# Optimization experiments

Hardware: AMD Instinct MI355X
Metric: run time of the kernel (lower is better)

The kernel has to match this reference:

```python
import jax, jax.numpy as jnp
import numpy as np

NUM_BREAKPOINTS = 100  # module default
IMG_SHAPE = (1, 1, 4096, 8192)  # B must be 1: PWL(num_channels=1) sees (C*H*W, B)


def setup_inputs() -> dict:
    key = jax.random.key(0)
    k1, k2, k3, k4 = jax.random.split(key, 4)
    x = jax.random.uniform(k1, IMG_SHAPE, dtype=jnp.float32)
    # torchpwl.PWL parameters (num_channels=1): breakpoint x-positions, per-segment
    # slopes, and bias (function value at the leftmost breakpoint).
    x_positions = jax.random.uniform(k2, (1, NUM_BREAKPOINTS), dtype=jnp.float32)
    slopes = 1.0 + 0.1 * jax.random.normal(k3, (1, NUM_BREAKPOINTS), dtype=jnp.float32)
    biases = 0.05 * jax.random.normal(k4, (1,), dtype=jnp.float32)
    return {"x": x, "x_positions": x_positions, "slopes": slopes, "biases": biases}


def _pwl(x_flat, x_positions, slopes, biases):
    # Sloped piecewise-linear function (torchpwl.BaseSlopedPWL math), 1 channel.
    # x_flat: (N,), x_positions/slopes: (1, K), biases: (1,)
    K = x_positions.shape[1]
    sorted_x = jnp.sort(x_positions, axis=1)                     # (1, K)
    skips = jnp.roll(sorted_x, -1, axis=1) - sorted_x            # last entry never used
    cumsums = jnp.cumsum(skips * slopes, axis=1)[:, :-1]         # (1, K-1)
    betas = jnp.concatenate([biases[:, None], biases[:, None] + cumsums], axis=1)  # (1, K)
    # segment index: (# breakpoints <= x) clamped to [1, K], minus 1
    idx = jnp.clip(jnp.searchsorted(sorted_x[0], x_flat, side="right"), 1, K) - 1
    return betas[0, idx] + (x_flat - sorted_x[0, idx]) * slopes[0, idx]


def reference(x, x_positions, slopes, biases):
    # forward: flatten -> PWL -> clip(0,1) -> reshape (original returns [out])
    y = _pwl(x.reshape(-1), x_positions, slopes, biases)
    return jnp.clip(y, 0.0, 1.0).reshape(x.shape)
```

## Files before the change

### kernel.cpp

```cpp
#include <hip/hip_runtime.h>

#define K  100
#define NB 1024

typedef float fvec4 __attribute__((ext_vector_type(4)));

__global__ __launch_bounds__(1024) void pwl_setup_kernel(
    const float* __restrict__ xp, const float* __restrict__ sl,
    const float* __restrict__ bias, float* __restrict__ a_g,
    float* __restrict__ b_g, float* __restrict__ sx_g,
    float2* __restrict__ ab_g) {
  __shared__ float s_pos[K];
  __shared__ float s_slope[K];
  __shared__ float s_x[K];
  __shared__ float s_c[K];
  __shared__ float s_sa[K];
  __shared__ float s_sb[K];
  __shared__ unsigned short s_cnt[NB + 1];
  const int t = threadIdx.x;

  if (t < K) { s_pos[t] = xp[t]; s_slope[t] = sl[t]; }
  __syncthreads();

  if (t < K) {
    float v = s_pos[t];
    int r = 0;
    for (int j = 0; j < K; ++j) {
      float u = s_pos[j];
      r += ((u < v) || (u == v && j < t)) ? 1 : 0;
    }
    s_x[r] = v;
  }
  __syncthreads();

  if (t < K - 1) s_c[t] = (s_x[t + 1] - s_x[t]) * s_slope[t];
  __syncthreads();
  for (int off = 1; off < K - 1; off <<= 1) {
    float v = 0.0f;
    if (t >= off && t < K - 1) v = s_c[t - off];
    __syncthreads();
    if (t < K - 1) s_c[t] += v;
    __syncthreads();
  }
  if (t < K) {
    float beta = bias[0] + (t ? s_c[t - 1] : 0.0f);
    float a = s_slope[t];
    s_sa[t] = a;
    s_sb[t] = beta - s_x[t] * a;
  }
  __syncthreads();

  if (t < K) {
    sx_g[t] = s_x[t];
    ab_g[t] = make_float2(s_sa[t], s_sb[t]);
  }

  for (int e = t; e <= NB; e += blockDim.x) {
    float ev = (float)e * (1.0f / (float)NB);
    int lo = 0, hi = K;
    while (lo < hi) {
      int mid = (lo + hi) >> 1;
      if (s_x[mid] <= ev) lo = mid + 1; else hi = mid;
    }
    s_cnt[e] = (unsigned short)lo;
  }
  __syncthreads();

  for (int b = t; b < NB; b += blockDim.x) {
    int lo = s_cnt[b], hi = s_cnt[b + 1];
    float av, bv;
    if (lo == hi) {
      int idx = min(max(lo, 1), K) - 1;
      av = s_sa[idx];
      bv = s_sb[idx];
    } else {
      av = __builtin_huge_valf();
      bv = __uint_as_float((unsigned)lo | ((unsigned)hi << 16));
    }
    a_g[b] = av;
    b_g[b] = bv;
  }
}

__device__ __forceinline__ float pwl_eval(float xv,
                                          const float* __restrict__ s_a,
                                          const float* __restrict__ s_b,
                                          const float* __restrict__ s_x,
                                          const float2* __restrict__ s_ab) {
  int bkt = (int)(xv * (float)NB);
  bkt = min(max(bkt, 0), NB - 1);
  float a = s_a[bkt];
  float b = s_b[bkt];
  if (__float_as_uint(a) == 0x7f800000u) {
    unsigned p = __float_as_uint(b);
    int lo = (int)(p & 0xffffu);
    int hi = (int)(p >> 16);
    while (lo < hi) {
      int mid = (lo + hi) >> 1;
      if (s_x[mid] <= xv) lo = mid + 1; else hi = mid;
    }
    int idx = min(max(lo, 1), K) - 1;
    float2 ab = s_ab[idx];
    a = ab.x;
    b = ab.y;
  }
  float y = fmaf(xv, a, b);
  return fminf(fmaxf(y, 0.0f), 1.0f);
}

__global__ __launch_bounds__(256) void pwl_main_kernel(
    const fvec4* __restrict__ x, const float* __restrict__ a_g,
    const float* __restrict__ b_g, const float* __restrict__ sx_g,
    const float2* __restrict__ ab_g, fvec4* __restrict__ out, int n4, int n) {
  __shared__ float s_a[NB];
  __shared__ float s_b[NB];
  __shared__ float s_x[K];
  __shared__ float2 s_ab[K];
  for (int i = threadIdx.x; i < NB; i += blockDim.x) {
    s_a[i] = a_g[i];
    s_b[i] = b_g[i];
  }
  if (threadIdx.x < K) {
    s_x[threadIdx.x] = sx_g[threadIdx.x];
    s_ab[threadIdx.x] = ab_g[threadIdx.x];
  }
  __syncthreads();

  const int stride = gridDim.x * blockDim.x;
  int i = blockIdx.x * blockDim.x + threadIdx.x;
  if (i < n4) {
    fvec4 v = x[i];
    while (true) {
      int inext = i + stride;
      bool more = inext < n4;
      fvec4 vn = {};
      if (more) vn = x[inext];
      fvec4 r;
      r.x = pwl_eval(v.x, s_a, s_b, s_x, s_ab);
      r.y = pwl_eval(v.y, s_a, s_b, s_x, s_ab);
      r.z = pwl_eval(v.z, s_a, s_b, s_x, s_ab);
      r.w = pwl_eval(v.w, s_a, s_b, s_x, s_ab);
      __builtin_nontemporal_store(r, &out[i]);
      if (!more) break;
      v = vn;
      i = inext;
    }
  }

  if (blockIdx.x == 0) {
    const float* xs = (const float*)x;
    float* os = (float*)out;
    for (int j = (n4 << 2) + threadIdx.x; j < n; j += blockDim.x) {
      os[j] = pwl_eval(xs[j], s_a, s_b, s_x, s_ab);
    }
  }
}

extern "C" void kernel_launch(void* const* d_in, const int* in_sizes, int n_in,
                              void* d_out, int out_size, void* d_ws, size_t ws_size,
                              hipStream_t stream) {
  const float* x    = (const float*)d_in[0];
  const float* xp   = (const float*)d_in[1];
  const float* sl   = (const float*)d_in[2];
  const float* bias = (const float*)d_in[3];
  float* out = (float*)d_out;

  float* a_tab = (float*)d_ws;
  float* b_tab = (float*)((char*)d_ws + NB * 4);
  float* sx    = (float*)((char*)d_ws + NB * 8);
  float2* ab   = (float2*)((char*)d_ws + NB * 8 + 512);

  const int n  = in_sizes[0];
  const int n4 = n >> 2;

  pwl_setup_kernel<<<1, 1024, 0, stream>>>(xp, sl, bias, a_tab, b_tab, sx, ab);

  const int threads = 256;
  const int blocks  = 2048;
  pwl_main_kernel<<<blocks, threads, 0, stream>>>(
      (const fvec4*)x, a_tab, b_tab, sx, ab, (fvec4*)out, n4, n);
}
```

Measured before the change: 243.0 us.

## Replace bucket table with branch-free two-breakpoint lookup and double-buffer loads

Each bucket now stores up to two breakpoint positions plus a base index packed into the low mantissa bits, so most lookups resolve with two comparisons. A global binary search is the fallback only for buckets holding more than two breakpoints. The old version did a shared-memory binary search whenever a bucket held any breakpoint. The main loop also keeps two vec4 loads in flight per iteration to deepen memory-level parallelism. The price is a slight truncation of breakpoint precision in the low mantissa bits and extra register pressure.

```diff
diff --git a/kernel.cpp b/kernel.cpp
--- a/kernel.cpp
+++ b/kernel.cpp
@@ -7,9 +7,9 @@
 
 __global__ __launch_bounds__(1024) void pwl_setup_kernel(
     const float* __restrict__ xp, const float* __restrict__ sl,
-    const float* __restrict__ bias, float* __restrict__ a_g,
-    float* __restrict__ b_g, float* __restrict__ sx_g,
-    float2* __restrict__ ab_g) {
+    const float* __restrict__ bias, float* __restrict__ s0_g,
+    float* __restrict__ s1_g, float* __restrict__ sa_g,
+    float* __restrict__ sb_g, float* __restrict__ sx_g) {
   __shared__ float s_pos[K];
   __shared__ float s_slope[K];
   __shared__ float s_x[K];
@@ -51,8 +51,9 @@
   __syncthreads();
 
   if (t < K) {
+    sa_g[t] = s_sa[t];
+    sb_g[t] = s_sb[t];
     sx_g[t] = s_x[t];
-    ab_g[t] = make_float2(s_sa[t], s_sb[t]);
   }
 
   for (int e = t; e <= NB; e += blockDim.x) {
@@ -68,82 +69,118 @@
 
   for (int b = t; b < NB; b += blockDim.x) {
     int lo = s_cnt[b], hi = s_cnt[b + 1];
-    float av, bv;
-    if (lo == hi) {
-      int idx = min(max(lo, 1), K) - 1;
-      av = s_sa[idx];
-      bv = s_sb[idx];
-    } else {
-      av = __builtin_huge_valf();
-      bv = __uint_as_float((unsigned)lo | ((unsigned)hi << 16));
-    }
-    a_g[b] = av;
-    b_g[b] = bv;
-  }
-}
-
-__device__ __forceinline__ float pwl_eval(float xv,
-                                          const float* __restrict__ s_a,
-                                          const float* __restrict__ s_b,
-                                          const float* __restrict__ s_x,
-                                          const float2* __restrict__ s_ab) {
-  int bkt = (int)(xv * (float)NB);
-  bkt = min(max(bkt, 0), NB - 1);
-  float a = s_a[bkt];
-  float b = s_b[bkt];
-  if (__float_as_uint(a) == 0x7f800000u) {
-    unsigned p = __float_as_uint(b);
-    int lo = (int)(p & 0xffffu);
-    int hi = (int)(p >> 16);
-    while (lo < hi) {
-      int mid = (lo + hi) >> 1;
-      if (s_x[mid] <= xv) lo = mid + 1; else hi = mid;
-    }
-    int idx = min(max(lo, 1), K) - 1;
-    float2 ab = s_ab[idx];
-    a = ab.x;
-    b = ab.y;
-  }
-  float y = fmaf(xv, a, b);
-  return fminf(fmaxf(y, 0.0f), 1.0f);
+    int m = hi - lo;
+    float s0 = (m >= 1) ? s_x[lo] : __builtin_huge_valf();
+    float s1 = (m >= 2) ? s_x[lo + 1] : __builtin_huge_valf();
+    unsigned enc = (unsigned)lo | ((m > 2) ? 0x80u : 0u);
+    unsigned u = (__float_as_uint(s0) & 0xFFFFFF00u) | enc;
+    s0_g[b] = __uint_as_float(u);
+    s1_g[b] = s1;
+  }
+}
+
+__device__ __forceinline__ int pwl_gsearch(const float* __restrict__ sx,
+                                           float xv) {
+  int lo = 0, hi = K;
+  while (lo < hi) {
+    int mid = (lo + hi) >> 1;
+    if (sx[mid] <= xv) lo = mid + 1; else hi = mid;
+  }
+  return max(lo - 1, 0);
+}
+
+__device__ __forceinline__ fvec4 pwl_eval4(fvec4 v,
+    const float* __restrict__ s_s0, const float* __restrict__ s_s1,
+    const float* __restrict__ s_sa, const float* __restrict__ s_sb,
+    const float* __restrict__ sx_g) {
+  int b0 = min(max((int)(v.x * (float)NB), 0), NB - 1);
+  int b1 = min(max((int)(v.y * (float)NB), 0), NB - 1);
+  int b2 = min(max((int)(v.z * (float)NB), 0), NB - 1);
+  int b3 = min(max((int)(v.w * (float)NB), 0), NB - 1);
+  unsigned u0 = __float_as_uint(s_s0[b0]);
+  unsigned u1 = __float_as_uint(s_s0[b1]);
+  unsigned u2 = __float_as_uint(s_s0[b2]);
+  unsigned u3 = __float_as_uint(s_s0[b3]);
+  float t0 = s_s1[b0], t1 = s_s1[b1], t2 = s_s1[b2], t3 = s_s1[b3];
+  int i0 = max((int)(u0 & 0x7fu) + (int)(v.x >= __uint_as_float(u0)) + (int)(v.x >= t0) - 1, 0);
+  int i1 = max((int)(u1 & 0x7fu) + (int)(v.y >= __uint_as_float(u1)) + (int)(v.y >= t1) - 1, 0);
+  int i2 = max((int)(u2 & 0x7fu) + (int)(v.z >= __uint_as_float(u2)) + (int)(v.z >= t2) - 1, 0);
+  int i3 = max((int)(u3 & 0x7fu) + (int)(v.w >= __uint_as_float(u3)) + (int)(v.w >= t3) - 1, 0);
+  if (__builtin_expect(((u0 | u1 | u2 | u3) & 0x80u) != 0, 0)) {
+    if (u0 & 0x80u) i0 = pwl_gsearch(sx_g, v.x);
+    if (u1 & 0x80u) i1 = pwl_gsearch(sx_g, v.y);
+    if (u2 & 0x80u) i2 = pwl_gsearch(sx_g, v.z);
+    if (u3 & 0x80u) i3 = pwl_gsearch(sx_g, v.w);
+  }
+  float a0 = s_sa[i0], a1 = s_sa[i1], a2 = s_sa[i2], a3 = s_sa[i3];
+  float c0 = s_sb[i0], c1 = s_sb[i1], c2 = s_sb[i2], c3 = s_sb[i3];
+  fvec4 r;
+  r.x = fminf(fmaxf(fmaf(v.x, a0, c0), 0.0f), 1.0f);
+  r.y = fminf(fmaxf(fmaf(v.y, a1, c1), 0.0f), 1.0f);
+  r.z = fminf(fmaxf(fmaf(v.z, a2, c2), 0.0f), 1.0f);
+  r.w = fminf(fmaxf(fmaf(v.w, a3, c3), 0.0f), 1.0f);
+  return r;
+}
+
+__device__ __forceinline__ float pwl_eval1(float xv,
+    const float* __restrict__ s_s0, const float* __restrict__ s_s1,
+    const float* __restrict__ s_sa, const float* __restrict__ s_sb,
+    const float* __restrict__ sx_g) {
+  int b = min(max((int)(xv * (float)NB), 0), NB - 1);
+  unsigned u = __float_as_uint(s_s0[b]);
+  float t = s_s1[b];
+  int idx = max((int)(u & 0x7fu) + (int)(xv >= __uint_as_float(u)) + (int)(xv >= t) - 1, 0);
+  if (__builtin_expect((u & 0x80u) != 0, 0)) idx = pwl_gsearch(sx_g, xv);
+  return fminf(fmaxf(fmaf(xv, s_sa[idx], s_sb[idx]), 0.0f), 1.0f);
 }
 
 __global__ __launch_bounds__(256) void pwl_main_kernel(
-    const fvec4* __restrict__ x, const float* __restrict__ a_g,
-    const float* __restrict__ b_g, const float* __restrict__ sx_g,
-    const float2* __restrict__ ab_g, fvec4* __restrict__ out, int n4, int n) {
-  __shared__ float s_a[NB];
-  __shared__ float s_b[NB];
-  __shared__ float s_x[K];
-  __shared__ float2 s_ab[K];
+    const fvec4* __restrict__ x, const float* __restrict__ s0_g,
+    const float* __restrict__ s1_g, const float* __restrict__ sa_g,
+    const float* __restrict__ sb_g, const float* __restrict__ sx_g,
+    fvec4* __restrict__ out, int n4, int n) {
+  __shared__ float s_s0[NB];
+  __shared__ float s_s1[NB];
+  __shared__ float s_sa[K];
+  __shared__ float s_sb[K];
   for (int i = threadIdx.x; i < NB; i += blockDim.x) {
-    s_a[i] = a_g[i];
-    s_b[i] = b_g[i];
+    s_s0[i] = s0_g[i];
+    s_s1[i] = s1_g[i];
   }
   if (threadIdx.x < K) {
-    s_x[threadIdx.x] = sx_g[threadIdx.x];
-    s_ab[threadIdx.x] = ab_g[threadIdx.x];
+    s_sa[threadIdx.x] = sa_g[threadIdx.x];
+    s_sb[threadIdx.x] = sb_g[threadIdx.x];
   }
   __syncthreads();
 
   const int stride = gridDim.x * blockDim.x;
   int i = blockIdx.x * blockDim.x + threadIdx.x;
   if (i < n4) {
-    fvec4 v = x[i];
+    fvec4 v0 = x[i];
+    int i1 = i + stride;
+    bool h1 = i1 < n4;
+    fvec4 v1 = {};
+    if (h1) v1 = x[i1];
     while (true) {
-      int inext = i + stride;
-      bool more = inext < n4;
-      fvec4 vn = {};
-      if (more) vn = x[inext];
-      fvec4 r;
-      r.x = pwl_eval(v.x, s_a, s_b, s_x, s_ab);
-      r.y = pwl_eval(v.y, s_a, s_b, s_x, s_ab);
-      r.z = pwl_eval(v.z, s_a, s_b, s_x, s_ab);
-      r.w = pwl_eval(v.w, s_a, s_b, s_x, s_ab);
-      __builtin_nontemporal_store(r, &out[i]);
-      if (!more) break;
-      v = vn;
-      i = inext;
+      int j0 = i + 2 * stride;
+      int j1 = i + 3 * stride;
+      bool g0 = j0 < n4;
+      bool g1 = j1 < n4;
+      fvec4 w0 = {}, w1 = {};
+      if (g0) w0 = x[j0];
+      if (g1) w1 = x[j1];
+
+      fvec4 r0 = pwl_eval4(v0, s_s0, s_s1, s_sa, s_sb, sx_g);
+      __builtin_nontemporal_store(r0, &out[i]);
+      if (h1) {
+        fvec4 r1 = pwl_eval4(v1, s_s0, s_s1, s_sa, s_sb, sx_g);
+        __builtin_nontemporal_store(r1, &out[i1]);
+      }
+
+      if (!g0) break;
+      i = j0; i1 = j1;
+      v0 = w0; v1 = w1;
+      h1 = g1;
     }
   }
 
@@ -151,7 +188,7 @@
     const float* xs = (const float*)x;
     float* os = (float*)out;
     for (int j = (n4 << 2) + threadIdx.x; j < n; j += blockDim.x) {
-      os[j] = pwl_eval(xs[j], s_a, s_b, s_x, s_ab);
+      os[j] = pwl_eval1(xs[j], s_s0, s_s1, s_sa, s_sb, sx_g);
     }
   }
 }
@@ -165,18 +202,19 @@
   const float* bias = (const float*)d_in[3];
   float* out = (float*)d_out;
 
-  float* a_tab = (float*)d_ws;
-  float* b_tab = (float*)((char*)d_ws + NB * 4);
-  float* sx    = (float*)((char*)d_ws + NB * 8);
-  float2* ab   = (float2*)((char*)d_ws + NB * 8 + 512);
+  float* s0 = (float*)d_ws;
+  float* s1 = (float*)((char*)d_ws + 4096);
+  float* sa = (float*)((char*)d_ws + 8192);
+  float* sb = (float*)((char*)d_ws + 8592);
+  float* sx = (float*)((char*)d_ws + 8992);
 
   const int n  = in_sizes[0];
   const int n4 = n >> 2;
 
-  pwl_setup_kernel<<<1, 1024, 0, stream>>>(xp, sl, bias, a_tab, b_tab, sx, ab);
+  pwl_setup_kernel<<<1, 1024, 0, stream>>>(xp, sl, bias, s0, s1, sa, sb, sx);
 
   const int threads = 256;
   const int blocks  = 2048;
   pwl_main_kernel<<<blocks, threads, 0, stream>>>(
-      (const fvec4*)x, a_tab, b_tab, sx, ab, (fvec4*)out, n4, n);
-}
+      (const fvec4*)x, s0, s1, sa, sb, sx, (fvec4*)out, n4, n);
+}
```

After: 257.6 us. 1.06x slower.
